# Optimization experiments

Hardware: AMD Instinct MI355X
Metric: run time of the kernel (lower is better)

The kernel has to match this reference:

```python
import jax, jax.numpy as jnp
import numpy as np

B, S, H, L, NH, F, V, K, R = 64, 512, 256, 4, 8, 1024, 50265, 8, 25
DH = H // NH
EPS = 1e-5


def layernorm(x, g, b):
    mu = x.mean(-1, keepdims=True)
    var = ((x - mu) ** 2).mean(-1, keepdims=True)
    return (x - mu) * jax.lax.rsqrt(var + EPS) * g + b


def setup_inputs() -> dict:
    key = jax.random.key(0)
    ks = jax.random.split(key, 24)
    input_ids = jax.random.randint(ks[0], (B, S), 0, V, dtype=jnp.int64)
    # prefix attention mask with variable valid lengths (ragged sequences)
    lengths = jax.random.randint(ks[1], (B,), 16, S + 1)
    attention_mask = (jnp.arange(S)[None, :] < lengths[:, None]).astype(jnp.int32)
    sub_indices = jax.random.randint(ks[2], (B, K), 0, S, dtype=jnp.int64)
    obj_indices = jax.random.randint(ks[3], (B, K), 0, S, dtype=jnp.int64)
    sub_counts = jax.random.randint(ks[4], (B,), 0, K + 1, dtype=jnp.int32)
    obj_counts = jax.random.randint(ks[5], (B,), 0, K + 1, dtype=jnp.int32)
    sc = 0.02
    p = {
        'emb': jax.random.normal(ks[6], (V, H), jnp.float32) * sc,
        'Wqkv': jax.random.normal(ks[7], (L, H, 3 * H), jnp.float32) * sc,
        'bqkv': jnp.zeros((L, 3 * H), jnp.float32),
        'Wo': jax.random.normal(ks[8], (L, H, H), jnp.float32) * sc,
        'bo': jnp.zeros((L, H), jnp.float32),
        'ln1_g': jnp.ones((L, H), jnp.float32), 'ln1_b': jnp.zeros((L, H), jnp.float32),
        'ln2_g': jnp.ones((L, H), jnp.float32), 'ln2_b': jnp.zeros((L, H), jnp.float32),
        'W1': jax.random.normal(ks[9], (L, H, F), jnp.float32) * sc,
        'b1': jnp.zeros((L, F), jnp.float32),
        'W2': jax.random.normal(ks[10], (L, F, H), jnp.float32) * sc,
        'b2': jnp.zeros((L, H), jnp.float32),
        'lnf_g': jnp.ones((H,), jnp.float32), 'lnf_b': jnp.zeros((H,), jnp.float32),
        'mW1': jax.random.normal(ks[11], (3 * H, H), jnp.float32) * sc,
        'mb1': jnp.zeros((H,), jnp.float32),
        'mW2': jax.random.normal(ks[12], (H, R), jnp.float32) * sc,
        'mb2': jnp.zeros((R,), jnp.float32),
    }
    return dict(input_ids=input_ids, attention_mask=attention_mask,
                sub_indices=sub_indices, sub_counts=sub_counts,
                obj_indices=obj_indices, obj_counts=obj_counts, **p)


def _encoder(input_ids, attention_mask, emb, Wqkv, bqkv, Wo, bo,
             ln1_g, ln1_b, ln2_g, ln2_b, W1, b1, W2, b2, lnf_g, lnf_b):
    x = emb[input_ids]  # [B,S,H]
    kbias = jnp.where(attention_mask[:, None, None, :] > 0, 0.0, -1e9)  # mask keys
    scale = 1.0 / np.sqrt(DH)
    for l in range(L):  # small fixed layer loop
        qkv = x @ Wqkv[l] + bqkv[l]
        q, k, v = jnp.split(qkv, 3, axis=-1)
        q = q.reshape(B, S, NH, DH).transpose(0, 2, 1, 3)
        k = k.reshape(B, S, NH, DH).transpose(0, 2, 1, 3)
        v = v.reshape(B, S, NH, DH).transpose(0, 2, 1, 3)
        scores = jnp.einsum('bhqd,bhkd->bhqk', q, k) * scale + kbias
        attn = jax.nn.softmax(scores, axis=-1)
        o = jnp.einsum('bhqk,bhkd->bhqd', attn, v).transpose(0, 2, 1, 3).reshape(B, S, H)
        x = layernorm(x + o @ Wo[l] + bo[l], ln1_g[l], ln1_b[l])
        h = jax.nn.relu(x @ W1[l] + b1[l]) @ W2[l] + b2[l]
        x = layernorm(x + h, ln2_g[l], ln2_b[l])
    return layernorm(x, lnf_g, lnf_b)


def _pooled(seq, idx, counts):
    g = jnp.take_along_axis(seq, idx[:, :, None], axis=1)  # [B,K,H]
    m = (jnp.arange(K)[None, :] < counts[:, None]).astype(seq.dtype)
    s = (g * m[:, :, None]).sum(1)
    c = counts.astype(seq.dtype)[:, None]
    return jnp.where(c > 0, s / jnp.maximum(c, 1.0), 0.0)  # zeros if no indices


def reference(input_ids, attention_mask, sub_indices, sub_counts, obj_indices, obj_counts,
              emb, Wqkv, bqkv, Wo, bo, ln1_g, ln1_b, ln2_g, ln2_b,
              W1, b1, W2, b2, lnf_g, lnf_b, mW1, mb1, mW2, mb2):
    seq = _encoder(input_ids, attention_mask, emb, Wqkv, bqkv, Wo, bo,
                   ln1_g, ln1_b, ln2_g, ln2_b, W1, b1, W2, b2, lnf_g, lnf_b)
    sub = _pooled(seq, sub_indices, sub_counts)
    obj = _pooled(seq, obj_indices, obj_counts)
    mask = attention_mask.astype(seq.dtype)
    lens = mask.sum(1)[:, None]
    story = jnp.where(lens > 0, (seq * mask[:, :, None]).sum(1) / jnp.maximum(lens, 1.0),
                      seq.mean(1))
    feat = jnp.concatenate([sub, obj, story], axis=-1)  # [B,3H]
    logits = jax.nn.relu(feat @ mW1 + mb1) @ mW2 + mb2
    return logits
```

## Files before the change

kernel.cpp:

```cpp
#include <hip/hip_runtime.h>
#include <hip/hip_bf16.h>


typedef __hip_bfloat16 bf16;
typedef __attribute__((ext_vector_type(8))) short short8;
typedef __attribute__((ext_vector_type(4))) float f32x4;

#define S_LEN 512
#define H_DIM 256
#define NTOK  32768
#define QSCALE 0.25503488f

__device__ __forceinline__ void gload_lds16(const void* g, void* l) {
  __builtin_amdgcn_global_load_lds(
      (const __attribute__((address_space(1))) unsigned int*)g,
      (__attribute__((address_space(3))) unsigned int*)l, 16, 0, 0);
}

__device__ __forceinline__ unsigned short f2bu(float x) {
  bf16 t = __float2bfloat16(x);
  return *reinterpret_cast<unsigned short*>(&t);
}
__device__ __forceinline__ float bu2f(unsigned short u) {
  unsigned int x = (unsigned int)u << 16;
  return __uint_as_float(x);
}

__global__ __launch_bounds__(64) void lens_kernel(
    const int* __restrict__ amask, int* __restrict__ ntiles,
    int* __restrict__ lenb) {
  const int b = blockIdx.x, t = threadIdx.x;
  int c = 0;
#pragma unroll
  for (int i = 0; i < 8; ++i) c += amask[b * S_LEN + t + i * 64];
#pragma unroll
  for (int off = 1; off < 64; off <<= 1) c += __shfl_xor(c, off);
  if (t == 0) {
    lenb[b] = c;
    ntiles[b] = (c + 63) >> 6;
  }
}

__global__ __launch_bounds__(64) void order_kernel(
    const int* __restrict__ ntiles, int* __restrict__ ordb) {
  const int b = threadIdx.x;
  const int ntb = ntiles[b];
  int rank = 0;
  for (int j = 0; j < 64; ++j) {
    const int ntj = __shfl(ntb, j);
    rank += (ntj > ntb) || (ntj == ntb && j < b);
  }
  ordb[rank] = b;
}

__global__ __launch_bounds__(256) void tcast_kernel(
    const float* __restrict__ in, bf16* __restrict__ out, int K, int N) {
  const int l = blockIdx.z;
  in  += (size_t)l * K * N;
  out += (size_t)l * K * N;
  __shared__ float t[32][33];
  const int n0 = blockIdx.x * 32, k0 = blockIdx.y * 32;
  const int c = threadIdx.x & 31, r = threadIdx.x >> 5;
#pragma unroll
  for (int rr = r; rr < 32; rr += 8)
    t[rr][c] = in[(size_t)(k0 + rr) * N + n0 + c];
  __syncthreads();
#pragma unroll
  for (int rr = r; rr < 32; rr += 8)
    out[(size_t)(n0 + rr) * K + k0 + c] = __float2bfloat16(t[c][rr]);
}

__global__ __launch_bounds__(256) void embed_kernel(
    const int* __restrict__ ids, const float* __restrict__ emb,
    bf16* __restrict__ Xb) {
  size_t i4 = (size_t)blockIdx.x * 256 + threadIdx.x;
  int tok = (int)(i4 >> 6);
  int d4  = (int)(i4 & 63);
  float4 v = *(const float4*)&emb[(size_t)ids[tok] * H_DIM + d4 * 4];
  ushort4 pk;
  pk.x = f2bu(v.x); pk.y = f2bu(v.y); pk.z = f2bu(v.z); pk.w = f2bu(v.w);
  *(ushort4*)&Xb[i4 * 4] = pk;
}

#define SRC_CHUNK(tid_) (((tid_) & 3) ^ (((tid_) >> 3) & 3))

template<int MODE, bool RELU>
__global__ __launch_bounds__(256) void hgemm_kernel(
    const bf16* __restrict__ A, const bf16* __restrict__ Bt,
    const float* __restrict__ bias, bf16* __restrict__ Cb,
    bf16* __restrict__ Kb, bf16* __restrict__ Vt,
    int M, int N, int K) {
  __shared__ __align__(16) bf16 Sh[16384];
  bf16* const As0 = Sh;
  bf16* const Bs0 = Sh + 8192;
  const int tid = threadIdx.x;
  const int wv = tid >> 6, ln = tid & 63;
  const int fr = ln & 15, g4 = ln >> 4;
  const int wr = wv >> 1, wc = wv & 1;
  const int m0 = blockIdx.x * 128, n0 = blockIdx.y * 128;
  const int lr = tid >> 2;
  const int lk = SRC_CHUNK(tid) * 8;
  const int rc = (g4 ^ ((fr >> 1) & 3)) * 8;

#define STAGE_G(buf, kk) do {                                                  \
    const int kof_ = (kk) * 32;                                                \
    gload_lds16(A  + (size_t)(m0 + lr) * K + kof_ + lk,                        \
                &As0[(buf) * 4096 + wv * 512]);                                \
    gload_lds16(A  + (size_t)(m0 + 64 + lr) * K + kof_ + lk,                   \
                &As0[(buf) * 4096 + 2048 + wv * 512]);                         \
    gload_lds16(Bt + (size_t)(n0 + lr) * K + kof_ + lk,                        \
                &Bs0[(buf) * 4096 + wv * 512]);                                \
    gload_lds16(Bt + (size_t)(n0 + 64 + lr) * K + kof_ + lk,                   \
                &Bs0[(buf) * 4096 + 2048 + wv * 512]);                         \
  } while (0)

  f32x4 acc[4][4];
#pragma unroll
  for (int i = 0; i < 4; ++i)
#pragma unroll
    for (int j = 0; j < 4; ++j)
      acc[i][j] = (f32x4){0.f, 0.f, 0.f, 0.f};

  const int NT = K >> 5;
  STAGE_G(0, 0);
  __syncthreads();
  int cur = 0;
  for (int kt = 0; kt < NT; ++kt) {
    if (kt + 1 < NT) STAGE_G(cur ^ 1, kt + 1);
    short8 af[4], bfv[4];
#pragma unroll
    for (int i = 0; i < 4; ++i)
      af[i] = *(const short8*)
          &As0[cur * 4096 + (wr * 64 + i * 16 + fr) * 32 + rc];
#pragma unroll
    for (int j = 0; j < 4; ++j)
      bfv[j] = *(const short8*)
          &Bs0[cur * 4096 + (wc * 64 + j * 16 + fr) * 32 + rc];
#pragma unroll
    for (int i = 0; i < 4; ++i)
#pragma unroll
      for (int j = 0; j < 4; ++j)
        acc[i][j] = __builtin_amdgcn_mfma_f32_16x16x32_bf16(
            af[i], bfv[j], acc[i][j], 0, 0, 0);
    __syncthreads();
    cur ^= 1;
  }
#undef STAGE_G

  const bool vpath = (MODE == 2) && (n0 >= 512);
#pragma unroll
  for (int j = 0; j < 4; ++j) {
    const int nl = wc * 64 + j * 16 + fr;
    const int n = n0 + nl;
    const float bv = bias[n];
    const float sc = (MODE == 2 && n < 256) ? QSCALE : 1.0f;
#pragma unroll
    for (int i = 0; i < 4; ++i) {
      const int mlb = wr * 64 + i * 16 + g4 * 4;
#pragma unroll
      for (int r = 0; r < 4; ++r) {
        float o = acc[i][j][r] + bv;
        if (RELU) o = fmaxf(o, 0.f);
        o *= sc;
        const int ml = mlb + r;
        const int addr = vpath ? nl * 128 + (ml ^ ((nl & 7) << 3))
                               : ml * 128 + (nl ^ ((ml & 7) << 3));
        Sh[addr] = __float2bfloat16(o);
      }
    }
  }
  __syncthreads();
  if (MODE == 1) {
#pragma unroll
    for (int p = 0; p < 8; ++p) {
      const int cid = p * 256 + tid;
      const int ml = cid >> 4, mc = cid & 15;
      const short8 v =
          *(const short8*)&Sh[ml * 128 + ((mc * 8) ^ ((ml & 7) << 3))];
      *(short8*)&Cb[(size_t)(m0 + ml) * N + n0 + mc * 8] = v;
    }
  } else if (!vpath) {
    const int bb = m0 >> 9, s0 = m0 & 511;
    const bool isK = (n0 >= 256);
    bf16* const dst = isK ? Kb : Cb;
    const int hbase = (n0 - (isK ? 256 : 0)) >> 5;
#pragma unroll
    for (int p = 0; p < 8; ++p) {
      const int cid = p * 256 + tid;
      const int ml = cid >> 4, mc = cid & 15;
      const short8 v =
          *(const short8*)&Sh[ml * 128 + ((mc * 8) ^ ((ml & 7) << 3))];
      const int hh = hbase + (mc >> 2);
      const int dd = (mc & 3) * 8;
      *(short8*)&dst[(((size_t)(bb * 8 + hh) * 512) + s0 + ml) * 32 + dd] = v;
    }
  } else {
    const int bb = m0 >> 9;
#pragma unroll
    for (int p = 0; p < 8; ++p) {
      const int cid = p * 256 + tid;
      const int ddl = cid >> 4, mc = cid & 15;
      const short8 v =
          *(const short8*)&Sh[ddl * 128 + ((mc * 8) ^ ((ddl & 7) << 3))];
      const int dd = (n0 - 512) + ddl;
      const int hh = dd >> 5, ddd = dd & 31;
      const int s8 = (m0 & 511) + mc * 8;
      const int ssw = (s8 & ~63) | ((s8 & 63) ^ ((ddd & 7) << 3));
      *(short8*)&Vt[(((size_t)bb * 8 + hh) * 32 + ddd) * 512 + ssw] = v;
    }
  }
}

template<bool OHEAD>
__global__ __launch_bounds__(256) void hgemm_ln_kernel(
    const bf16* __restrict__ A, const bf16* __restrict__ Bt,
    const float* __restrict__ bias, bf16* __restrict__ Xbf,
    const float* __restrict__ g, const float* __restrict__ bt, int K) {
  __shared__ __align__(16) bf16 Sh[20480];
  bf16* const As0 = Sh;
  bf16* const Bs0 = Sh + 4096;
  float* const rsum = (float*)Sh;
  float* const rsq  = (float*)(Sh + 512);
  bf16*  const XbT  = Sh + 1024;
  const int tid = threadIdx.x;
  const int wv = tid >> 6;
  const int ln = tid & 63;
  const int fr = ln & 15, g4 = ln >> 4;
  const int m0 = blockIdx.x * 64;
  const int rc = (g4 ^ ((fr >> 1) & 3)) * 8;

#define STAGE_L(buf, kk) do {                                                  \
    const int kof_ = (kk) * 32;                                                \
    if (OHEAD) {                                                               \
      gload_lds16(A + ((size_t)((m0 >> 9) * 8 + (kk)) * 512 + (m0 & 511) +     \
                       (tid >> 2)) * 32 + SRC_CHUNK(tid) * 8,                  \
                  &As0[(buf) * 2048 + wv * 512]);                              \
    } else {                                                                   \
      gload_lds16(A + (size_t)(m0 + (tid >> 2)) * K + kof_ +                   \
                      SRC_CHUNK(tid) * 8,                                      \
                  &As0[(buf) * 2048 + wv * 512]);                              \
    }                                                                          \
    _Pragma("unroll")                                                          \
    for (int e = 0; e < 4; ++e) {                                              \
      const int vt = e * 256 + tid;                                            \
      gload_lds16(Bt + (size_t)(vt >> 2) * K + kof_ + SRC_CHUNK(vt) * 8,       \
                  &Bs0[(buf) * 8192 + e * 2048 + wv * 512]);                   \
    }                                                                          \
  } while (0)

  f32x4 acc[4][4];
#pragma unroll
  for (int i = 0; i < 4; ++i)
#pragma unroll
    for (int j = 0; j < 4; ++j)
      acc[i][j] = (f32x4){0.f, 0.f, 0.f, 0.f};

  const int NT = K >> 5;
  STAGE_L(0, 0);
  __syncthreads();
  int cur = 0;
  for (int kt = 0; kt < NT; ++kt) {
    if (kt + 1 < NT) STAGE_L(cur ^ 1, kt + 1);
    short8 af[4], bfv[4];
#pragma unroll
    for (int i = 0; i < 4; ++i)
      af[i] = *(const short8*)&As0[cur * 2048 + (i * 16 + fr) * 32 + rc];
#pragma unroll
    for (int j = 0; j < 4; ++j)
      bfv[j] = *(const short8*)
          &Bs0[cur * 8192 + (wv * 64 + j * 16 + fr) * 32 + rc];
#pragma unroll
    for (int i = 0; i < 4; ++i)
#pragma unroll
      for (int j = 0; j < 4; ++j)
        acc[i][j] = __builtin_amdgcn_mfma_f32_16x16x32_bf16(
            af[i], bfv[j], acc[i][j], 0, 0, 0);
    __syncthreads();
    cur ^= 1;
  }
#undef STAGE_L

#pragma unroll
  for (int p = 0; p < 8; ++p) {
    const int seg = p * 4 + wv;
    gload_lds16(Xbf + (size_t)(m0 + seg * 2 + (ln >> 5)) * 256 +
                    (ln & 31) * 8,
                &XbT[seg * 512]);
  }
  __syncthreads();

  float gj[4], bj[4], bsj[4];
#pragma unroll
  for (int j = 0; j < 4; ++j) {
    const int n = wv * 64 + j * 16 + fr;
    gj[j] = g[n]; bj[j] = bt[n]; bsj[j] = bias[n];
  }
#pragma unroll
  for (int i = 0; i < 4; ++i) {
#pragma unroll
    for (int r = 0; r < 4; ++r) {
      const int ml = i * 16 + g4 * 4 + r;
#pragma unroll
      for (int j = 0; j < 4; ++j) {
        const int nl = wv * 64 + j * 16 + fr;
        acc[i][j][r] += bsj[j] +
            bu2f(*(const unsigned short*)&XbT[ml * 256 + nl]);
      }
    }
  }
#pragma unroll
  for (int i = 0; i < 4; ++i) {
#pragma unroll
    for (int r = 0; r < 4; ++r) {
      float sp = acc[i][0][r] + acc[i][1][r] + acc[i][2][r] + acc[i][3][r];
      float qp = acc[i][0][r] * acc[i][0][r] + acc[i][1][r] * acc[i][1][r] +
                 acc[i][2][r] * acc[i][2][r] + acc[i][3][r] * acc[i][3][r];
#pragma unroll
      for (int off = 1; off < 16; off <<= 1) {
        sp += __shfl_xor(sp, off);
        qp += __shfl_xor(qp, off);
      }
      if (fr == 0) {
        const int ri = i * 16 + g4 * 4 + r;
        rsum[wv * 64 + ri] = sp;
        rsq[wv * 64 + ri] = qp;
      }
    }
  }
  __syncthreads();
#pragma unroll
  for (int i = 0; i < 4; ++i) {
#pragma unroll
    for (int r = 0; r < 4; ++r) {
      const int ri = i * 16 + g4 * 4 + r;
      const float tot = rsum[ri] + rsum[64 + ri] + rsum[128 + ri] +
                        rsum[192 + ri];
      const float tq = rsq[ri] + rsq[64 + ri] + rsq[128 + ri] + rsq[192 + ri];
      const float mu = tot * (1.0f / 256.0f);
      const float var = tq * (1.0f / 256.0f) - mu * mu;
      const float rstd = rsqrtf(var + 1e-5f);
#pragma unroll
      for (int j = 0; j < 4; ++j) {
        const int nl = wv * 64 + j * 16 + fr;
        const float o = (acc[i][j][r] - mu) * rstd * gj[j] + bj[j];
        XbT[ri * 256 + (nl ^ ((ri & 7) << 3))] = __float2bfloat16(o);
      }
    }
  }
  __syncthreads();
#pragma unroll
  for (int p = 0; p < 8; ++p) {
    const int c8 = p * 256 + tid;
    const int row = c8 >> 5, cc = c8 & 31;
    const short8 v =
        *(const short8*)&XbT[row * 256 + ((cc * 8) ^ ((row & 7) << 3))];
    *(short8*)&Xbf[(size_t)(m0 + row) * 256 + cc * 8] = v;
  }
}

__global__ __launch_bounds__(512, 8) void attn_mfma_kernel(
    const bf16* __restrict__ Qh, const bf16* __restrict__ Kh,
    const bf16* __restrict__ Vt,
    const int* __restrict__ amask, const int* __restrict__ ntiles,
    const int* __restrict__ ordb, bf16* __restrict__ Ob) {
  const int b = ordb[blockIdx.z];
  const int h = blockIdx.x;
  const int qg = blockIdx.y;
  const int tid = threadIdx.x;
  const int wv = tid >> 6, ln = tid & 63;
  const int fr = ln & 15, g4 = ln >> 4;
  const int f8 = (fr & 7) << 3;
  const int rc = (g4 ^ ((fr >> 1) & 3)) * 8;
  const size_t bh512 = (size_t)(b * 8 + h) * 512;
  const int bh32 = (b * 8 + h) * 32;
  __shared__ __align__(16) bf16 Ks[2][2048];
  __shared__ __align__(16) bf16 Vs[2][2048];
  __shared__ __align__(16) bf16 Ps[8192];
  __shared__ __align__(16) float Ms[64];

  const int nt = ntiles[b];

  if (tid < 64)
    Ms[tid] = (amask[b * S_LEN + (nt - 1) * 64 + tid] != 0) ? 0.f : -1e9f;

  const int tv = tid & 255;
  const bf16* gK = Kh + (bh512 + (tv >> 2)) * 32 + SRC_CHUNK(tv) * 8;
  const bf16* gV = Vt + (size_t)(bh32 + (tv >> 3)) * 512 + (tv & 7) * 8;

#define STAGE_A2(buf) do {                                                     \
    if (tid < 256) gload_lds16(gK, &Ks[(buf)][(tv >> 6) * 512]);               \
    else           gload_lds16(gV, &Vs[(buf)][(tv >> 6) * 512]);               \
  } while (0)

  gload_lds16(Qh + (bh512 + qg * 128 + (tid >> 2)) * 32 + SRC_CHUNK(tid) * 8,
              &Ps[wv * 512]);
  STAGE_A2(0);
  __syncthreads();
  const short8 qb = *(const short8*)&Ps[wv * 512 + fr * 32 + rc];
  __syncthreads();

  f32x4 accO[2];
  accO[0] = (f32x4){0.f, 0.f, 0.f, 0.f};
  accO[1] = (f32x4){0.f, 0.f, 0.f, 0.f};
  float mrun = -1e30f, lrun = 0.f;
  const int srcq = 20 * g4;

#define SOFTMAX_PV(CURBUF)                                                     \
  do {                                                                         \
    const float a0 = fmaxf(fmaxf(p[0], p[1]), p[2]);                           \
    const float a1 = fmaxf(fmaxf(p[3], p[4]), p[5]);                           \
    const float a2 = fmaxf(fmaxf(p[6], p[7]), p[8]);                           \
    const float a3 = fmaxf(fmaxf(p[9], p[10]), p[11]);                         \
    const float a4 = fmaxf(fmaxf(p[12], p[13]), p[14]);                        \
    float mx = fmaxf(fmaxf(fmaxf(a0, a1), fmaxf(a2, a3)),                      \
                     fmaxf(a4, p[15]));                                        \
    mx = fmaxf(mx, __shfl_xor(mx, 16));                                        \
    mx = fmaxf(mx, __shfl_xor(mx, 32));                                        \
    float corr = 1.f;                                                          \
    if (!__all(mx <= mrun + 8.f)) {                                            \
      const float mnew = fmaxf(mrun, mx);                                      \
      corr = exp2f(mrun - mnew);                                               \
      mrun = mnew;                                                             \
      _Pragma("unroll")                                                        \
      for (int rr = 0; rr < 4; ++rr) {                                         \
        const float cs = __shfl(corr, srcq + rr);                              \
        accO[0][rr] *= cs;                                                     \
        accO[1][rr] *= cs;                                                     \
      }                                                                        \
    }                                                                          \
    _Pragma("unroll")                                                          \
    for (int i = 0; i < 16; ++i) p[i] = exp2f(p[i] - mrun);                    \
    const float s0_ = p[0] + p[1], s1_ = p[2] + p[3], s2_ = p[4] + p[5],       \
                s3_ = p[6] + p[7], s4_ = p[8] + p[9], s5_ = p[10] + p[11],     \
                s6_ = p[12] + p[13], s7_ = p[14] + p[15];                      \
    float ps = ((s0_ + s1_) + (s2_ + s3_)) + ((s4_ + s5_) + (s6_ + s7_));      \
    ps += __shfl_xor(ps, 16);                                                  \
    ps += __shfl_xor(ps, 32);                                                  \
    lrun = lrun * corr + ps;                                                   \
    _Pragma("unroll")                                                          \
    for (int kb = 0; kb < 4; ++kb) {                                           \
      ushort4 w4;                                                              \
      w4.x = f2bu(p[kb * 4 + 0]);                                              \
      w4.y = f2bu(p[kb * 4 + 1]);                                              \
      w4.z = f2bu(p[kb * 4 + 2]);                                              \
      w4.w = f2bu(p[kb * 4 + 3]);                                              \
      *(ushort4*)&Ps[wv * 1024 + fr * 64 + ((kb * 16 + g4 * 4) ^ f8)] = w4;    \
    }                                                                          \
    _Pragma("unroll")                                                          \
    for (int kk = 0; kk < 2; ++kk) {                                           \
      const short8 pa = *(const short8*)                                       \
          &Ps[wv * 1024 + fr * 64 + ((kk * 32 + g4 * 8) ^ f8)];                \
      _Pragma("unroll")                                                        \
      for (int df = 0; df < 2; ++df) {                                         \
        const short8 vb = *(const short8*)                                     \
            &Vs[CURBUF][(df * 16 + fr) * 64 + ((kk * 32 + g4 * 8) ^ f8)];      \
        accO[df] = __builtin_amdgcn_mfma_f32_16x16x32_bf16(                    \
            pa, vb, accO[df], 0, 0, 0);                                        \
      }                                                                        \
    }                                                                          \
  } while (0)

  int cur = 0;
  for (int kt = 0; kt < nt - 1; ++kt) {
    gK += 64 * 32;
    gV += 64;
    STAGE_A2(cur ^ 1);

    f32x4 st[4];
#pragma unroll
    for (int kb = 0; kb < 4; ++kb) {
      const short8 kf = *(const short8*)&Ks[cur][(kb * 16 + fr) * 32 + rc];
      f32x4 z = (f32x4){0.f, 0.f, 0.f, 0.f};
      st[kb] = __builtin_amdgcn_mfma_f32_16x16x32_bf16(kf, qb, z, 0, 0, 0);
    }
    float p[16];
#pragma unroll
    for (int kb = 0; kb < 4; ++kb)
#pragma unroll
      for (int rr = 0; rr < 4; ++rr) p[kb * 4 + rr] = st[kb][rr];

    SOFTMAX_PV(cur);
    __syncthreads();
    cur ^= 1;
  }

  {
    f32x4 st[4];
#pragma unroll
    for (int kb = 0; kb < 4; ++kb) {
      const short8 kf = *(const short8*)&Ks[cur][(kb * 16 + fr) * 32 + rc];
      f32x4 z = (f32x4){0.f, 0.f, 0.f, 0.f};
      st[kb] = __builtin_amdgcn_mfma_f32_16x16x32_bf16(kf, qb, z, 0, 0, 0);
    }
    float p[16];
#pragma unroll
    for (int kb = 0; kb < 4; ++kb) {
      const f32x4 mv = ((const f32x4*)Ms)[kb * 4 + g4];
#pragma unroll
      for (int rr = 0; rr < 4; ++rr) p[kb * 4 + rr] = st[kb][rr] + mv[rr];
    }
    SOFTMAX_PV(cur);
  }
#undef SOFTMAX_PV
#undef STAGE_A2

  const float inv = 1.0f / lrun;
#pragma unroll
  for (int rr = 0; rr < 4; ++rr) {
    const float iv = __shfl(inv, srcq + rr);
    const int q = qg * 128 + wv * 16 + g4 * 4 + rr;
    const size_t orow = (bh512 + q) * 32;
    Ob[orow + fr]      = __float2bfloat16(accO[0][rr] * iv);
    Ob[orow + 16 + fr] = __float2bfloat16(accO[1][rr] * iv);
  }
}

__global__ __launch_bounds__(256) void lnf_pool_kernel(
    bf16* __restrict__ Xbf, const float* __restrict__ g,
    const float* __restrict__ bt, const int* __restrict__ amask,
    float* __restrict__ Pstory) {
  const int b = blockIdx.x, sg = blockIdx.y;
  const int tid = threadIdx.x, wv = tid >> 6, ln = tid & 63;
  const float4 gg = ((const float4*)g)[ln];
  const float4 bb = ((const float4*)bt)[ln];
  float ax = 0.f, ay = 0.f, az = 0.f, aw = 0.f;
  for (int t = wv; t < 64; t += 4) {
    const size_t tok = (size_t)b * S_LEN + sg * 64 + t;
    const ushort4 u = *(const ushort4*)&Xbf[tok * 256 + ln * 4];
    const float vx = bu2f(u.x), vy = bu2f(u.y), vz = bu2f(u.z),
                vw = bu2f(u.w);
    float s = vx + vy + vz + vw;
#pragma unroll
    for (int off = 1; off < 64; off <<= 1) s += __shfl_xor(s, off);
    const float mu = s * (1.0f / 256.0f);
    const float dx = vx - mu, dy = vy - mu, dz = vz - mu, dw = vw - mu;
    float sq = dx * dx + dy * dy + dz * dz + dw * dw;
#pragma unroll
    for (int off = 1; off < 64; off <<= 1) sq += __shfl_xor(sq, off);
    const float rstd = rsqrtf(sq * (1.0f / 256.0f) + 1e-5f);
    const float ox = dx * rstd * gg.x + bb.x;
    const float oy = dy * rstd * gg.y + bb.y;
    const float oz = dz * rstd * gg.z + bb.z;
    const float ow = dw * rstd * gg.w + bb.w;
    ushort4 o4;
    o4.x = f2bu(ox); o4.y = f2bu(oy); o4.z = f2bu(oz); o4.w = f2bu(ow);
    *(ushort4*)&Xbf[tok * 256 + ln * 4] = o4;
    if (amask[tok]) { ax += ox; ay += oy; az += oz; aw += ow; }
  }
  __shared__ float part[4][256];
  part[wv][ln * 4 + 0] = ax;
  part[wv][ln * 4 + 1] = ay;
  part[wv][ln * 4 + 2] = az;
  part[wv][ln * 4 + 3] = aw;
  __syncthreads();
  const float tot = part[0][tid] + part[1][tid] + part[2][tid] + part[3][tid];
  Pstory[((size_t)b * 8 + sg) * 256 + tid] = tot;
}

__global__ __launch_bounds__(1024) void poolcls_kernel(
    const bf16* __restrict__ Xbf, const float* __restrict__ Pstory,
    const int* __restrict__ lenb,
    const int* __restrict__ sub_idx, const int* __restrict__ sub_cnt,
    const int* __restrict__ obj_idx, const int* __restrict__ obj_cnt,
    const float* __restrict__ mW1, const float* __restrict__ mb1,
    const float* __restrict__ mW2, const float* __restrict__ mb2,
    float* __restrict__ out) {
  const int b = blockIdx.x, tid = threadIdx.x;
  const int t = tid & 255, sl = tid >> 8;
  __shared__ float fs[768];
  __shared__ float part[4][256];
  __shared__ float hid[256];
  __shared__ float w2s[256 * 25];
  const bf16* xb = Xbf + (size_t)b * S_LEN * H_DIM;
  for (int i = tid; i < 6400; i += 1024) w2s[i] = mW2[i];
  if (sl == 0) {
    float s = 0.f;
#pragma unroll
    for (int i = 0; i < 8; ++i) s += Pstory[((size_t)b * 8 + i) * 256 + t];
    fs[512 + t] = s / (float)lenb[b];
  } else if (sl == 1) {
    const int cc = sub_cnt[b];
    float s2 = 0.f;
    for (int j = 0; j < cc; ++j)
      s2 += __bfloat162float(xb[(size_t)sub_idx[b * 8 + j] * H_DIM + t]);
    fs[t] = (cc > 0) ? s2 / (float)cc : 0.f;
  } else if (sl == 2) {
    const int cc = obj_cnt[b];
    float s2 = 0.f;
    for (int j = 0; j < cc; ++j)
      s2 += __bfloat162float(xb[(size_t)obj_idx[b * 8 + j] * H_DIM + t]);
    fs[256 + t] = (cc > 0) ? s2 / (float)cc : 0.f;
  }
  __syncthreads();
  float acc = 0.f;
  for (int k = sl * 192; k < sl * 192 + 192; ++k)
    acc += fs[k] * mW1[(size_t)k * 256 + t];
  part[sl][t] = acc;
  __syncthreads();
  if (sl == 0)
    hid[t] = fmaxf(part[0][t] + part[1][t] + part[2][t] + part[3][t] +
                       mb1[t],
                   0.f);
  __syncthreads();
  if (tid < 25) {
    float o = mb2[tid];
    for (int j = 0; j < 256; ++j) o += hid[j] * w2s[j * 25 + tid];
    out[b * 25 + tid] = o;
  }
}

extern "C" void kernel_launch(void* const* d_in, const int* in_sizes, int n_in,
                              void* d_out, int out_size, void* d_ws, size_t ws_size,
                              hipStream_t stream) {
  const int*   input_ids = (const int*)d_in[0];
  const int*   amask     = (const int*)d_in[1];
  const int*   sub_idx   = (const int*)d_in[2];
  const int*   sub_cnt   = (const int*)d_in[3];
  const int*   obj_idx   = (const int*)d_in[4];
  const int*   obj_cnt   = (const int*)d_in[5];
  const float* emb  = (const float*)d_in[6];
  const float* Wqkv = (const float*)d_in[7];
  const float* bqkv = (const float*)d_in[8];
  const float* Wo   = (const float*)d_in[9];
  const float* bo   = (const float*)d_in[10];
  const float* ln1g = (const float*)d_in[11];
  const float* ln1b = (const float*)d_in[12];
  const float* ln2g = (const float*)d_in[13];
  const float* ln2b = (const float*)d_in[14];
  const float* W1   = (const float*)d_in[15];
  const float* b1   = (const float*)d_in[16];
  const float* W2   = (const float*)d_in[17];
  const float* b2   = (const float*)d_in[18];
  const float* lnfg = (const float*)d_in[19];
  const float* lnfb = (const float*)d_in[20];
  const float* mW1  = (const float*)d_in[21];
  const float* mb1  = (const float*)d_in[22];
  const float* mW2  = (const float*)d_in[23];
  const float* mb2  = (const float*)d_in[24];
  float* out = (float*)d_out;

  char* w = (char*)d_ws;
  bf16*  Xb   = (bf16*)w;                          w += (size_t)NTOK * 256 * 2;
  bf16*  Qh   = (bf16*)w;                          w += (size_t)NTOK * 256 * 2;
  bf16*  Kh   = (bf16*)w;                          w += (size_t)NTOK * 256 * 2;
  bf16*  Vtg  = (bf16*)w;                          w += (size_t)NTOK * 256 * 2;
  bf16*  Ob   = (bf16*)w;                          w += (size_t)NTOK * 256 * 2;
  bf16*  Wqkvt= (bf16*)w;                          w += (size_t)4 * 768 * 256 * 2;
  bf16*  Wot  = (bf16*)w;                          w += (size_t)4 * 256 * 256 * 2;
  bf16*  W1t  = (bf16*)w;                          w += (size_t)4 * 1024 * 256 * 2;
  bf16*  W2t  = (bf16*)w;                          w += (size_t)4 * 256 * 1024 * 2;
  float* Pstory = (float*)w;                       w += (size_t)64 * 8 * 256 * 4;
  int*   ntiles = (int*)w;                         w += 256;
  int*   lenb   = (int*)w;                         w += 256;
  int*   ordb   = (int*)w;                         w += 256;
  bf16*  Hb   = Qh;

  lens_kernel<<<64, 64, 0, stream>>>(amask, ntiles, lenb);
  order_kernel<<<1, 64, 0, stream>>>(ntiles, ordb);
  tcast_kernel<<<dim3(24, 8, 4), 256, 0, stream>>>(Wqkv, Wqkvt, 256, 768);
  tcast_kernel<<<dim3(8, 8, 4), 256, 0, stream>>>(Wo, Wot, 256, 256);
  tcast_kernel<<<dim3(32, 8, 4), 256, 0, stream>>>(W1, W1t, 256, 1024);
  tcast_kernel<<<dim3(8, 32, 4), 256, 0, stream>>>(W2, W2t, 1024, 256);

  embed_kernel<<<8192, 256, 0, stream>>>(input_ids, emb, Xb);

  for (int l = 0; l < 4; ++l) {
    const bf16* Wqkvt_l = Wqkvt + (size_t)l * 768 * 256;
    const bf16* Wot_l   = Wot + (size_t)l * 256 * 256;
    const bf16* W1t_l   = W1t + (size_t)l * 1024 * 256;
    const bf16* W2t_l   = W2t + (size_t)l * 256 * 1024;

    hgemm_kernel<2, false><<<dim3(256, 6), 256, 0, stream>>>(
        Xb, Wqkvt_l, bqkv + (size_t)l * 768, Qh, Kh, Vtg, NTOK, 768, 256);
    attn_mfma_kernel<<<dim3(8, 4, 64), 512, 0, stream>>>(
        Qh, Kh, Vtg, amask, ntiles, ordb, Ob);
    hgemm_ln_kernel<true><<<512, 256, 0, stream>>>(
        Ob, Wot_l, bo + (size_t)l * 256, Xb,
        ln1g + l * 256, ln1b + l * 256, 256);
    hgemm_kernel<1, true><<<dim3(256, 8), 256, 0, stream>>>(
        Xb, W1t_l, b1 + (size_t)l * 1024, Hb, nullptr, nullptr,
        NTOK, 1024, 256);
    hgemm_ln_kernel<false><<<512, 256, 0, stream>>>(
        Hb, W2t_l, b2 + (size_t)l * 256, Xb,
        ln2g + l * 256, ln2b + l * 256, 1024);
  }
  lnf_pool_kernel<<<dim3(64, 8), 256, 0, stream>>>(Xb, lnfg, lnfb, amask,
                                                   Pstory);
  poolcls_kernel<<<64, 1024, 0, stream>>>(Xb, Pstory, lenb, sub_idx, sub_cnt,
                                          obj_idx, obj_cnt, mW1, mb1, mW2, mb2,
                                          out);
}
```

Baseline: 679.0 us.

## Run FFN down-projection in FP8 with FP8 hidden activations and scaled weights

The FFN up-projection GEMM now writes its ReLU output as FP8 e4m3 instead of bf16, and W2 is transposed and quantized to FP8 with a fixed scale. A new fused GEMM+LayerNorm kernel uses the fp8 MFMA 16x16x32 instruction over K=1024 and undoes the weight scale in the epilogue. This halves the bytes of the hidden activation written and read, and raises MFMA throughput for the largest GEMM. In exchange it loses accuracy from the FP8 activations and weights, with no per-tensor calibration.

```diff
diff --git a/kernel.cpp b/kernel.cpp
--- a/kernel.cpp
+++ b/kernel.cpp
@@ -1,15 +1,19 @@
 #include <hip/hip_runtime.h>
 #include <hip/hip_bf16.h>
+#include <hip/hip_fp8.h>
 
 
 typedef __hip_bfloat16 bf16;
 typedef __attribute__((ext_vector_type(8))) short short8;
 typedef __attribute__((ext_vector_type(4))) float f32x4;
+typedef unsigned char u8;
 
 #define S_LEN 512
 #define H_DIM 256
 #define NTOK  32768
 #define QSCALE 0.25503488f
+#define W2SCALE 64.0f
+#define INV_W2SCALE 0.015625f
 
 __device__ __forceinline__ void gload_lds16(const void* g, void* l) {
   __builtin_amdgcn_global_load_lds(
@@ -24,6 +28,10 @@
 __device__ __forceinline__ float bu2f(unsigned short u) {
   unsigned int x = (unsigned int)u << 16;
   return __uint_as_float(x);
+}
+__device__ __forceinline__ u8 f2fp8(float x) {
+  __hip_fp8_e4m3 t(x);
+  return (u8)t.__x;
 }
 
 __global__ __launch_bounds__(64) void lens_kernel(
@@ -68,6 +76,23 @@
 #pragma unroll
   for (int rr = r; rr < 32; rr += 8)
     out[(size_t)(n0 + rr) * K + k0 + c] = __float2bfloat16(t[c][rr]);
+}
+
+__global__ __launch_bounds__(256) void tcast8_kernel(
+    const float* __restrict__ in, u8* __restrict__ out, int K, int N) {
+  const int l = blockIdx.z;
+  in  += (size_t)l * K * N;
+  out += (size_t)l * K * N;
+  __shared__ float t[32][33];
+  const int n0 = blockIdx.x * 32, k0 = blockIdx.y * 32;
+  const int c = threadIdx.x & 31, r = threadIdx.x >> 5;
+#pragma unroll
+  for (int rr = r; rr < 32; rr += 8)
+    t[rr][c] = in[(size_t)(k0 + rr) * N + n0 + c];
+  __syncthreads();
+#pragma unroll
+  for (int rr = r; rr < 32; rr += 8)
+    out[(size_t)(n0 + rr) * K + k0 + c] = f2fp8(t[c][rr] * W2SCALE);
 }
 
 __global__ __launch_bounds__(256) void embed_kernel(
@@ -88,11 +113,12 @@
 __global__ __launch_bounds__(256) void hgemm_kernel(
     const bf16* __restrict__ A, const bf16* __restrict__ Bt,
     const float* __restrict__ bias, bf16* __restrict__ Cb,
-    bf16* __restrict__ Kb, bf16* __restrict__ Vt,
+    bf16* __restrict__ Kb, bf16* __restrict__ Vt, u8* __restrict__ C8,
     int M, int N, int K) {
   __shared__ __align__(16) bf16 Sh[16384];
   bf16* const As0 = Sh;
   bf16* const Bs0 = Sh + 8192;
+  u8*   const ShB = (u8*)Sh;
   const int tid = threadIdx.x;
   const int wv = tid >> 6, ln = tid & 63;
   const int fr = ln & 15, g4 = ln >> 4;
@@ -163,21 +189,26 @@
         if (RELU) o = fmaxf(o, 0.f);
         o *= sc;
         const int ml = mlb + r;
-        const int addr = vpath ? nl * 128 + (ml ^ ((nl & 7) << 3))
-                               : ml * 128 + (nl ^ ((ml & 7) << 3));
-        Sh[addr] = __float2bfloat16(o);
+        if (MODE == 3) {
+          const int swzc = (nl >> 4) ^ (ml & 7);
+          ShB[ml * 128 + swzc * 16 + (nl & 15)] = f2fp8(o);
+        } else {
+          const int addr = vpath ? nl * 128 + (ml ^ ((nl & 7) << 3))
+                                 : ml * 128 + (nl ^ ((ml & 7) << 3));
+          Sh[addr] = __float2bfloat16(o);
+        }
       }
     }
   }
   __syncthreads();
-  if (MODE == 1) {
-#pragma unroll
-    for (int p = 0; p < 8; ++p) {
+  if (MODE == 3) {
+#pragma unroll
+    for (int p = 0; p < 4; ++p) {
       const int cid = p * 256 + tid;
-      const int ml = cid >> 4, mc = cid & 15;
-      const short8 v =
-          *(const short8*)&Sh[ml * 128 + ((mc * 8) ^ ((ml & 7) << 3))];
-      *(short8*)&Cb[(size_t)(m0 + ml) * N + n0 + mc * 8] = v;
+      const int row = cid >> 3, mc = cid & 7;
+      const uint4 v =
+          *(const uint4*)&ShB[row * 128 + ((mc ^ (row & 7)) * 16)];
+      *(uint4*)&C8[(size_t)(m0 + row) * N + n0 + mc * 16] = v;
     }
   } else if (!vpath) {
     const int bb = m0 >> 9, s0 = m0 & 511;
@@ -304,6 +335,146 @@
       for (int j = 0; j < 4; ++j) {
         const int nl = wv * 64 + j * 16 + fr;
         acc[i][j][r] += bsj[j] +
+            bu2f(*(const unsigned short*)&XbT[ml * 256 + nl]);
+      }
+    }
+  }
+#pragma unroll
+  for (int i = 0; i < 4; ++i) {
+#pragma unroll
+    for (int r = 0; r < 4; ++r) {
+      float sp = acc[i][0][r] + acc[i][1][r] + acc[i][2][r] + acc[i][3][r];
+      float qp = acc[i][0][r] * acc[i][0][r] + acc[i][1][r] * acc[i][1][r] +
+                 acc[i][2][r] * acc[i][2][r] + acc[i][3][r] * acc[i][3][r];
+#pragma unroll
+      for (int off = 1; off < 16; off <<= 1) {
+        sp += __shfl_xor(sp, off);
+        qp += __shfl_xor(qp, off);
+      }
+      if (fr == 0) {
+        const int ri = i * 16 + g4 * 4 + r;
+        rsum[wv * 64 + ri] = sp;
+        rsq[wv * 64 + ri] = qp;
+      }
+    }
+  }
+  __syncthreads();
+#pragma unroll
+  for (int i = 0; i < 4; ++i) {
+#pragma unroll
+    for (int r = 0; r < 4; ++r) {
+      const int ri = i * 16 + g4 * 4 + r;
+      const float tot = rsum[ri] + rsum[64 + ri] + rsum[128 + ri] +
+                        rsum[192 + ri];
+      const float tq = rsq[ri] + rsq[64 + ri] + rsq[128 + ri] + rsq[192 + ri];
+      const float mu = tot * (1.0f / 256.0f);
+      const float var = tq * (1.0f / 256.0f) - mu * mu;
+      const float rstd = rsqrtf(var + 1e-5f);
+#pragma unroll
+      for (int j = 0; j < 4; ++j) {
+        const int nl = wv * 64 + j * 16 + fr;
+        const float o = (acc[i][j][r] - mu) * rstd * gj[j] + bj[j];
+        XbT[ri * 256 + (nl ^ ((ri & 7) << 3))] = __float2bfloat16(o);
+      }
+    }
+  }
+  __syncthreads();
+#pragma unroll
+  for (int p = 0; p < 8; ++p) {
+    const int c8 = p * 256 + tid;
+    const int row = c8 >> 5, cc = c8 & 31;
+    const short8 v =
+        *(const short8*)&XbT[row * 256 + ((cc * 8) ^ ((row & 7) << 3))];
+    *(short8*)&Xbf[(size_t)(m0 + row) * 256 + cc * 8] = v;
+  }
+}
+
+__global__ __launch_bounds__(256) void hgemm_ln8_kernel(
+    const u8* __restrict__ A8, const u8* __restrict__ B8,
+    const float* __restrict__ bias, bf16* __restrict__ Xbf,
+    const float* __restrict__ g, const float* __restrict__ bt) {
+  __shared__ __align__(16) u8 Sh8[34816];
+  u8*    const As8 = Sh8;
+  u8*    const Bs8 = Sh8 + 4096;
+  float* const rsum = (float*)Sh8;
+  float* const rsq  = (float*)(Sh8 + 1024);
+  bf16*  const XbT  = (bf16*)(Sh8 + 2048);
+  const int tid = threadIdx.x;
+  const int wv = tid >> 6;
+  const int ln = tid & 63;
+  const int fr = ln & 15, g4 = ln >> 4;
+  const int m0 = blockIdx.x * 64;
+  const int K = 1024;
+
+#define STAGE_F8(buf, kk) do {                                                 \
+    const int kof_ = (kk) * 32;                                                \
+    if (tid < 128)                                                             \
+      gload_lds16(A8 + (size_t)(m0 + (tid >> 1)) * K + kof_ + (tid & 1) * 16,  \
+                  &As8[(buf) * 2048 + tid * 16]);                              \
+    _Pragma("unroll")                                                          \
+    for (int e = 0; e < 2; ++e) {                                              \
+      const int cid = e * 256 + tid;                                           \
+      gload_lds16(B8 + (size_t)(cid >> 1) * K + kof_ + (cid & 1) * 16,         \
+                  &Bs8[(buf) * 8192 + cid * 16]);                              \
+    }                                                                          \
+  } while (0)
+
+  f32x4 acc[4][4];
+#pragma unroll
+  for (int i = 0; i < 4; ++i)
+#pragma unroll
+    for (int j = 0; j < 4; ++j)
+      acc[i][j] = (f32x4){0.f, 0.f, 0.f, 0.f};
+
+  const int NT = 32;
+  STAGE_F8(0, 0);
+  __syncthreads();
+  int cur = 0;
+  for (int kt = 0; kt < NT; ++kt) {
+    if (kt + 1 < NT) STAGE_F8(cur ^ 1, kt + 1);
+    long af[4], bfv[4];
+#pragma unroll
+    for (int i = 0; i < 4; ++i)
+      af[i] = *(const long*)&As8[cur * 2048 + (i * 16 + fr) * 32 + g4 * 8];
+#pragma unroll
+    for (int j = 0; j < 4; ++j)
+      bfv[j] = *(const long*)
+          &Bs8[cur * 8192 + (wv * 64 + j * 16 + fr) * 32 + g4 * 8];
+#pragma unroll
+    for (int i = 0; i < 4; ++i)
+#pragma unroll
+      for (int j = 0; j < 4; ++j)
+        acc[i][j] = __builtin_amdgcn_mfma_f32_16x16x32_fp8_fp8(
+            af[i], bfv[j], acc[i][j], 0, 0, 0);
+    __syncthreads();
+    cur ^= 1;
+  }
+#undef STAGE_F8
+
+#pragma unroll
+  for (int p = 0; p < 8; ++p) {
+    const int seg = p * 4 + wv;
+    gload_lds16(Xbf + (size_t)(m0 + seg * 2 + (ln >> 5)) * 256 +
+                    (ln & 31) * 8,
+                &XbT[seg * 512]);
+  }
+  __syncthreads();
+
+  float gj[4], bj[4], bsj[4];
+#pragma unroll
+  for (int j = 0; j < 4; ++j) {
+    const int n = wv * 64 + j * 16 + fr;
+    gj[j] = g[n]; bj[j] = bt[n]; bsj[j] = bias[n];
+  }
+#pragma unroll
+  for (int i = 0; i < 4; ++i) {
+#pragma unroll
+    for (int r = 0; r < 4; ++r) {
+      const int ml = i * 16 + g4 * 4 + r;
+#pragma unroll
+      for (int j = 0; j < 4; ++j) {
+        const int nl = wv * 64 + j * 16 + fr;
+        acc[i][j][r] = acc[i][j][r] * INV_W2SCALE + bsj[j] +
             bu2f(*(const unsigned short*)&XbT[ml * 256 + nl]);
       }
     }
@@ -648,19 +819,19 @@
   bf16*  Wqkvt= (bf16*)w;                          w += (size_t)4 * 768 * 256 * 2;
   bf16*  Wot  = (bf16*)w;                          w += (size_t)4 * 256 * 256 * 2;
   bf16*  W1t  = (bf16*)w;                          w += (size_t)4 * 1024 * 256 * 2;
-  bf16*  W2t  = (bf16*)w;                          w += (size_t)4 * 256 * 1024 * 2;
+  u8*    W2t8 = (u8*)w;                            w += (size_t)4 * 256 * 1024;
   float* Pstory = (float*)w;                       w += (size_t)64 * 8 * 256 * 4;
   int*   ntiles = (int*)w;                         w += 256;
   int*   lenb   = (int*)w;                         w += 256;
   int*   ordb   = (int*)w;                         w += 256;
-  bf16*  Hb   = Qh;
+  u8*    H8   = (u8*)Qh;
 
   lens_kernel<<<64, 64, 0, stream>>>(amask, ntiles, lenb);
   order_kernel<<<1, 64, 0, stream>>>(ntiles, ordb);
   tcast_kernel<<<dim3(24, 8, 4), 256, 0, stream>>>(Wqkv, Wqkvt, 256, 768);
   tcast_kernel<<<dim3(8, 8, 4), 256, 0, stream>>>(Wo, Wot, 256, 256);
   tcast_kernel<<<dim3(32, 8, 4), 256, 0, stream>>>(W1, W1t, 256, 1024);
-  tcast_kernel<<<dim3(8, 32, 4), 256, 0, stream>>>(W2, W2t, 1024, 256);
+  tcast8_kernel<<<dim3(8, 32, 4), 256, 0, stream>>>(W2, W2t8, 1024, 256);
 
   embed_kernel<<<8192, 256, 0, stream>>>(input_ids, emb, Xb);
 
@@ -668,21 +839,22 @@
     const bf16* Wqkvt_l = Wqkvt + (size_t)l * 768 * 256;
     const bf16* Wot_l   = Wot + (size_t)l * 256 * 256;
     const bf16* W1t_l   = W1t + (size_t)l * 1024 * 256;
-    const bf16* W2t_l   = W2t + (size_t)l * 256 * 1024;
+    const u8*   W2t8_l  = W2t8 + (size_t)l * 256 * 1024;
 
     hgemm_kernel<2, false><<<dim3(256, 6), 256, 0, stream>>>(
-        Xb, Wqkvt_l, bqkv + (size_t)l * 768, Qh, Kh, Vtg, NTOK, 768, 256);
+        Xb, Wqkvt_l, bqkv + (size_t)l * 768, Qh, Kh, Vtg, nullptr,
+        NTOK, 768, 256);
     attn_mfma_kernel<<<dim3(8, 4, 64), 512, 0, stream>>>(
         Qh, Kh, Vtg, amask, ntiles, ordb, Ob);
     hgemm_ln_kernel<true><<<512, 256, 0, stream>>>(
         Ob, Wot_l, bo + (size_t)l * 256, Xb,
         ln1g + l * 256, ln1b + l * 256, 256);
-    hgemm_kernel<1, true><<<dim3(256, 8), 256, 0, stream>>>(
-        Xb, W1t_l, b1 + (size_t)l * 1024, Hb, nullptr, nullptr,
+    hgemm_kernel<3, true><<<dim3(256, 8), 256, 0, stream>>>(
+        Xb, W1t_l, b1 + (size_t)l * 1024, nullptr, nullptr, nullptr, H8,
         NTOK, 1024, 256);
-    hgemm_ln_kernel<false><<<512, 256, 0, stream>>>(
-        Hb, W2t_l, b2 + (size_t)l * 256, Xb,
-        ln2g + l * 256, ln2b + l * 256, 1024);
+    hgemm_ln8_kernel<<<512, 256, 0, stream>>>(
+        H8, W2t8_l, b2 + (size_t)l * 256, Xb,
+        ln2g + l * 256, ln2b + l * 256);
   }
   lnf_pool_kernel<<<dim3(64, 8), 256, 0, stream>>>(Xb, lnfg, lnfb, amask,
                                                    Pstory);
```

New measurement: 716.0 us. 1.05x slower.
